# Optimization experiments

Measured on AMD Instinct MI355X. Metric: run time of the kernel, lower is better.

Reference implementation:

```python
import jax, jax.numpy as jnp
import numpy as np

N_NODES = 50000
N_EDGES = 600000
IN_DIM = 9
HID = 128
OUT_DIM = 6


def _mlp2(x, W1, b1, W2, b2):
    # Linear -> ReLU -> Linear
    h = jax.nn.relu(x @ W1 + b1)
    return h @ W2 + b2


def setup_inputs() -> dict:
    key = jax.random.key(0)
    ks = jax.random.split(key, 16)

    def lin(k, fan_in, fan_out):
        # torch nn.Linear default init: U(-1/sqrt(fan_in), 1/sqrt(fan_in))
        bound = 1.0 / np.sqrt(fan_in)
        kw, kb = jax.random.split(k)
        W = jax.random.uniform(kw, (fan_in, fan_out), jnp.float32, -bound, bound)
        b = jax.random.uniform(kb, (fan_out,), jnp.float32, -bound, bound)
        return W, b

    node_states = jax.random.normal(ks[0], (N_NODES, IN_DIM), jnp.float32)
    edge_index = jax.random.randint(ks[1], (2, N_EDGES), 0, N_NODES, jnp.int64 if jax.config.jax_enable_x64 else jnp.int32)
    edge_attr = jax.random.uniform(ks[2], (N_EDGES, 1), jnp.float32)

    ne_W1, ne_b1 = lin(ks[3], IN_DIM, HID)
    ne_W2, ne_b2 = lin(ks[4], HID, HID)
    ee_W1, ee_b1 = lin(ks[5], 2 * HID + 1, HID)
    ee_W2, ee_b2 = lin(ks[6], HID, HID)
    nu_W1, nu_b1 = lin(ks[7], 2 * HID, HID)
    nu_W2, nu_b2 = lin(ks[8], HID, OUT_DIM)

    return {
        "node_states": node_states, "edge_index": edge_index, "edge_attr": edge_attr,
        "ne_W1": ne_W1, "ne_b1": ne_b1, "ne_W2": ne_W2, "ne_b2": ne_b2,
        "ee_W1": ee_W1, "ee_b1": ee_b1, "ee_W2": ee_W2, "ee_b2": ee_b2,
        "nu_W1": nu_W1, "nu_b1": nu_b1, "nu_W2": nu_W2, "nu_b2": nu_b2,
    }


def reference(node_states, edge_index, edge_attr,
              ne_W1, ne_b1, ne_W2, ne_b2,
              ee_W1, ee_b1, ee_W2, ee_b2,
              nu_W1, nu_b1, nu_W2, nu_b2):
    num_nodes = node_states.shape[0]
    # node encoder: [N, 9] -> [N, 128]
    h_v = _mlp2(node_states, ne_W1, ne_b1, ne_W2, ne_b2)

    row, col = edge_index[0], edge_index[1]
    # gather endpoints + concat edge features: [E, 257]
    edge_inputs = jnp.concatenate([h_v[row], h_v[col], edge_attr], axis=1)
    h_e = _mlp2(edge_inputs, ee_W1, ee_b1, ee_W2, ee_b2)  # [E, 128]

    # scatter-add messages to destination nodes (index_add_ on col)
    agg_messages = jax.ops.segment_sum(h_e, col, num_segments=num_nodes)  # [N, 128]

    node_inputs = jnp.concatenate([h_v, agg_messages], axis=1)  # [N, 256]
    gnn_deltas = _mlp2(node_inputs, nu_W1, nu_b1, nu_W2, nu_b2)  # [N, 6]
    return gnn_deltas
```

## Files before the change

kernel.cpp:

```cpp
#include <hip/hip_runtime.h>

#define N_NODES 50000
#define N_EDGES 600000
#define IN_DIM 9
#define HID 128
#define OUT_DIM 6
#define SCAN_BLKS ((N_NODES + 255) / 256)

typedef __attribute__((ext_vector_type(8))) short short8;
typedef __attribute__((ext_vector_type(4))) float f32x4;

__device__ __forceinline__ void split_bf16(float x, ushort& hi, ushort& lo) {
    unsigned u = __float_as_uint(x);
    unsigned r = u + 0x7FFF + ((u >> 16) & 1);
    hi = (ushort)(r >> 16);
    float hif = __uint_as_float((unsigned)hi << 16);
    lo = (ushort)(__float_as_uint(x - hif) >> 16);
}

__global__ __launch_bounds__(128)
void node_encoder(const float* __restrict__ x,
                  const float* __restrict__ W1, const float* __restrict__ b1,
                  const float* __restrict__ W2, const float* __restrict__ b2,
                  ushort* __restrict__ hvh, ushort* __restrict__ hvl)
{
    const int t  = threadIdx.x;
    const int n0 = blockIdx.x * 4;

    __shared__ float xs[4][12];
    __shared__ float h1[4][132];

    if (t < 4 * IN_DIM) {
        int n = t / IN_DIM, k = t % IN_DIM;
        xs[n][k] = x[(n0 + n) * IN_DIM + k];
    }
    __syncthreads();

    float w[IN_DIM];
#pragma unroll
    for (int k = 0; k < IN_DIM; ++k) w[k] = W1[k * HID + t];
    const float bb1 = b1[t];
#pragma unroll
    for (int n = 0; n < 4; ++n) {
        float s = bb1;
#pragma unroll
        for (int k = 0; k < IN_DIM; ++k) s += xs[n][k] * w[k];
        h1[n][t] = fmaxf(s, 0.f);
    }
    __syncthreads();

    float acc[4] = {0.f, 0.f, 0.f, 0.f};
    for (int k = 0; k < HID; k += 4) {
        const float w0 = W2[(k + 0) * HID + t];
        const float w1 = W2[(k + 1) * HID + t];
        const float w2 = W2[(k + 2) * HID + t];
        const float w3 = W2[(k + 3) * HID + t];
#pragma unroll
        for (int n = 0; n < 4; ++n) {
            const float4 a = *(const float4*)&h1[n][k];
            acc[n] += a.x * w0 + a.y * w1 + a.z * w2 + a.w * w3;
        }
    }
    const float bb2 = b2[t];
#pragma unroll
    for (int n = 0; n < 4; ++n) {
        ushort hi, lo;
        split_bf16(acc[n] + bb2, hi, lo);
        hvh[(size_t)(n0 + n) * HID + t] = hi;
        hvl[(size_t)(n0 + n) * HID + t] = lo;
    }
}

__global__ __launch_bounds__(256)
void csr_count(const int* __restrict__ col, int* __restrict__ cnt) {
    const int i = blockIdx.x * 256 + threadIdx.x;
    if (i < N_EDGES) atomicAdd(&cnt[col[i]], 1);
}

__global__ __launch_bounds__(256)
void scan_part(const int* __restrict__ cnt, int* __restrict__ part) {
    __shared__ int s[256];
    const int tid = threadIdx.x;
    const int i = blockIdx.x * 256 + tid;
    s[tid] = (i < N_NODES) ? cnt[i] : 0;
    __syncthreads();
#pragma unroll
    for (int off = 128; off > 0; off >>= 1) {
        if (tid < off) s[tid] += s[tid + off];
        __syncthreads();
    }
    if (tid == 0) part[blockIdx.x] = s[0];
}

__global__ __launch_bounds__(256)
void scan_scan(int* __restrict__ part) {
    __shared__ int s[256];
    const int tid = threadIdx.x;
    const int v = (tid < SCAN_BLKS) ? part[tid] : 0;
    s[tid] = v;
    __syncthreads();
    for (int off = 1; off < 256; off <<= 1) {
        int x = (tid >= off) ? s[tid - off] : 0;
        __syncthreads();
        s[tid] += x;
        __syncthreads();
    }
    part[tid] = s[tid] - v;
}

__global__ __launch_bounds__(256)
void scan_final(const int* __restrict__ cnt, const int* __restrict__ part,
                int* __restrict__ ofs, int* __restrict__ cursor) {
    __shared__ int s[256];
    const int tid = threadIdx.x;
    const int i = blockIdx.x * 256 + tid;
    const int v = (i < N_NODES) ? cnt[i] : 0;
    s[tid] = v;
    __syncthreads();
    for (int off = 1; off < 256; off <<= 1) {
        int x = (tid >= off) ? s[tid - off] : 0;
        __syncthreads();
        s[tid] += x;
        __syncthreads();
    }
    const int excl = part[blockIdx.x] + s[tid] - v;
    if (i <= N_NODES) ofs[i] = excl;
    if (i <  N_NODES) cursor[i] = excl;
}

__global__ __launch_bounds__(256)
void csr_fill(const int* __restrict__ col, int* __restrict__ cursor,
              int* __restrict__ eid) {
    const int i = blockIdx.x * 256 + threadIdx.x;
    if (i < N_EDGES) {
        const int p = atomicAdd(&cursor[col[i]], 1);
        eid[p] = i;
    }
}

__global__ __launch_bounds__(64)
void pack_weights(const float* __restrict__ W1, const float* __restrict__ W2,
                  ushort* __restrict__ p1h, ushort* __restrict__ p1l,
                  ushort* __restrict__ p2h, ushort* __restrict__ p2l)
{
    const int l = threadIdx.x;
    const int b = blockIdx.x;
    if (b < 64) {
        const int kt = b >> 3, nt = b & 7;
        const int kbase = kt * 32 + 8 * (l >> 4);
        const int n = nt * 16 + (l & 15);
#pragma unroll
        for (int j = 0; j < 8; ++j) {
            ushort hi, lo;
            split_bf16(W1[(kbase + j) * HID + n], hi, lo);
            p1h[(b * 64 + l) * 8 + j] = hi;
            p1l[(b * 64 + l) * 8 + j] = lo;
        }
    } else {
        const int u = b - 64;
        const int kt = u >> 3, nt = u & 7;
        const int kbase = kt * 32 + 8 * (l >> 4);
        const int n = nt * 16 + (l & 15);
#pragma unroll
        for (int j = 0; j < 8; ++j) {
            ushort hi, lo;
            split_bf16(W2[(kbase + j) * HID + n], hi, lo);
            p2h[(u * 64 + l) * 8 + j] = hi;
            p2l[(u * 64 + l) * 8 + j] = lo;
        }
    }
}

__global__ __launch_bounds__(256, 8)
void edge_mfma(const ushort* __restrict__ hvh, const ushort* __restrict__ hvl,
               const int* __restrict__ row, const int* __restrict__ col,
               const float* __restrict__ eattr,
               const int* __restrict__ eids,
               const ushort* __restrict__ p1h, const ushort* __restrict__ p1l,
               const ushort* __restrict__ p2h, const ushort* __restrict__ p2l,
               const float* __restrict__ W1,
               const float* __restrict__ b1, const float* __restrict__ b2,
               float* __restrict__ agg)
{
    __shared__ __align__(16) ushort H1h[4096];
    __shared__ __align__(16) ushort H1l[4096];
    __shared__ int   rows_s[32], cols_s[32];
    __shared__ float attr_s[32];

    const int tid = threadIdx.x;
    const int e0  = blockIdx.x * 32;

    if (tid < 32) {
        const int e = eids[e0 + tid];
        rows_s[tid] = row[e];
        cols_s[tid] = col[e];
        attr_s[tid] = eattr[e];
    }
    __syncthreads();

    const int l  = tid & 63;
    const int w  = tid >> 6;
    const int h  = w & 1;
    const int nh = w >> 1;
    const int gl = l >> 4;
    const int r  = l & 15;

    const int edge  = h * 16 + r;
    const int rbyte = rows_s[edge] * 256 + gl * 16;
    const int cbyte = cols_s[edge] * 256 + gl * 16;

    f32x4 acc[4] = {{0,0,0,0},{0,0,0,0},{0,0,0,0},{0,0,0,0}};
#pragma unroll
    for (int kt = 0; kt < 8; ++kt) {
        const int off = (kt < 4) ? (rbyte + kt * 64) : (cbyte + (kt - 4) * 64);
        const short8 ah = *(const short8*)((const char*)hvh + off);
        const short8 al = *(const short8*)((const char*)hvl + off);
#pragma unroll
        for (int i = 0; i < 4; ++i) {
            const int nt = nh * 4 + i;
            const short8 bh = *(const short8*)&p1h[((kt * 8 + nt) * 64 + l) * 8];
            const short8 bl = *(const short8*)&p1l[((kt * 8 + nt) * 64 + l) * 8];
            acc[i] = __builtin_amdgcn_mfma_f32_16x16x32_bf16(ah, bh, acc[i], 0, 0, 0);
            acc[i] = __builtin_amdgcn_mfma_f32_16x16x32_bf16(ah, bl, acc[i], 0, 0, 0);
            acc[i] = __builtin_amdgcn_mfma_f32_16x16x32_bf16(al, bh, acc[i], 0, 0, 0);
        }
    }

#pragma unroll
    for (int i = 0; i < 4; ++i) {
        const int ncol = nh * 64 + i * 16 + r;
        const float w256 = W1[256 * HID + ncol];
        const float bb   = b1[ncol];
        const int kt2 = ncol >> 5;
        const int g2  = (ncol >> 3) & 3;
        const int j   = ncol & 7;
#pragma unroll
        for (int q = 0; q < 4; ++q) {
            const int er = gl * 4 + q;
            const float a = attr_s[h * 16 + er];
            float v = fmaxf(acc[i][q] + bb + a * w256, 0.f);
            ushort hi, lo;
            split_bf16(v, hi, lo);
            const int cell = (kt2 * 2 + h) * 64 + g2 * 16 + er;
            H1h[cell * 8 + j] = hi;
            H1l[cell * 8 + j] = lo;
        }
    }
    __syncthreads();

    f32x4 acc2[4] = {{0,0,0,0},{0,0,0,0},{0,0,0,0},{0,0,0,0}};
#pragma unroll
    for (int kt = 0; kt < 4; ++kt) {
        const short8 ah = *(const short8*)&H1h[((kt * 2 + h) * 64 + l) * 8];
        const short8 al = *(const short8*)&H1l[((kt * 2 + h) * 64 + l) * 8];
#pragma unroll
        for (int i = 0; i < 4; ++i) {
            const int nt = nh * 4 + i;
            const short8 bh = *(const short8*)&p2h[((kt * 8 + nt) * 64 + l) * 8];
            const short8 bl = *(const short8*)&p2l[((kt * 8 + nt) * 64 + l) * 8];
            acc2[i] = __builtin_amdgcn_mfma_f32_16x16x32_bf16(ah, bh, acc2[i], 0, 0, 0);
            acc2[i] = __builtin_amdgcn_mfma_f32_16x16x32_bf16(ah, bl, acc2[i], 0, 0, 0);
            acc2[i] = __builtin_amdgcn_mfma_f32_16x16x32_bf16(al, bh, acc2[i], 0, 0, 0);
        }
    }

    const int er0 = h * 16 + gl * 4;
    const int n0s = cols_s[er0 + 0];
    const int n1s = cols_s[er0 + 1];
    const int n2s = cols_s[er0 + 2];
    const int n3s = cols_s[er0 + 3];
#pragma unroll
    for (int i = 0; i < 4; ++i) {
        const int ncol = nh * 64 + i * 16 + r;
        const float bb = b2[ncol];
        const float v0 = acc2[i][0] + bb;
        const float v1 = acc2[i][1] + bb;
        const float v2 = acc2[i][2] + bb;
        const float v3 = acc2[i][3] + bb;
        if (n0s == n3s) {
            atomicAdd(&agg[(size_t)n0s * HID + ncol], v0 + v1 + v2 + v3);
        } else {
            atomicAdd(&agg[(size_t)n0s * HID + ncol], v0);
            atomicAdd(&agg[(size_t)n1s * HID + ncol], v1);
            atomicAdd(&agg[(size_t)n2s * HID + ncol], v2);
            atomicAdd(&agg[(size_t)n3s * HID + ncol], v3);
        }
    }
}

__global__ __launch_bounds__(128)
void node_update(const ushort* __restrict__ hvh, const ushort* __restrict__ hvl,
                 const float* __restrict__ agg,
                 const float* __restrict__ W1, const float* __restrict__ b1,
                 const float* __restrict__ W2, const float* __restrict__ b2,
                 float* __restrict__ out)
{
    const int t  = threadIdx.x;
    const int n0 = blockIdx.x * 4;

    __shared__ float ins[4][260];
    __shared__ float h1[4][132];
    __shared__ float part[4][2][6];

#pragma unroll
    for (int n = 0; n < 4; ++n) {
        const unsigned hh = hvh[(size_t)(n0 + n) * HID + t];
        const unsigned ll = hvl[(size_t)(n0 + n) * HID + t];
        ins[n][t]       = __uint_as_float(hh << 16) + __uint_as_float(ll << 16);
        ins[n][HID + t] = agg[(size_t)(n0 + n) * HID + t];
    }
    __syncthreads();

    float acc[4] = {0.f, 0.f, 0.f, 0.f};
    for (int k = 0; k < 2 * HID; k += 4) {
        const float w0 = W1[(k + 0) * HID + t];
        const float w1 = W1[(k + 1) * HID + t];
        const float w2 = W1[(k + 2) * HID + t];
        const float w3 = W1[(k + 3) * HID + t];
#pragma unroll
        for (int n = 0; n < 4; ++n) {
            const float4 a = *(const float4*)&ins[n][k];
            acc[n] += a.x * w0 + a.y * w1 + a.z * w2 + a.w * w3;
        }
    }
    const float bb1 = b1[t];
#pragma unroll
    for (int n = 0; n < 4; ++n) h1[n][t] = fmaxf(acc[n] + bb1, 0.f);
    __syncthreads();

    float wv[6];
#pragma unroll
    for (int j = 0; j < 6; ++j) wv[j] = W2[t * OUT_DIM + j];

#pragma unroll
    for (int n = 0; n < 4; ++n) {
        const float v = h1[n][t];
        float p[6];
#pragma unroll
        for (int j = 0; j < 6; ++j) p[j] = v * wv[j];
#pragma unroll
        for (int off = 32; off > 0; off >>= 1) {
#pragma unroll
            for (int j = 0; j < 6; ++j) p[j] += __shfl_down(p[j], off);
        }
        if ((t & 63) == 0) {
#pragma unroll
            for (int j = 0; j < 6; ++j) part[n][t >> 6][j] = p[j];
        }
    }
    __syncthreads();

    if (t < 24) {
        const int n = t / 6, j = t % 6;
        out[(size_t)(n0 + n) * OUT_DIM + j] = part[n][0][j] + part[n][1][j] + b2[j];
    }
}

extern "C" void kernel_launch(void* const* d_in, const int* in_sizes, int n_in,
                              void* d_out, int out_size, void* d_ws, size_t ws_size,
                              hipStream_t stream) {
    const float* node_states = (const float*)d_in[0];
    const int*   edge_index  = (const int*)d_in[1];
    const float* edge_attr   = (const float*)d_in[2];
    const float* ne_W1 = (const float*)d_in[3];
    const float* ne_b1 = (const float*)d_in[4];
    const float* ne_W2 = (const float*)d_in[5];
    const float* ne_b2 = (const float*)d_in[6];
    const float* ee_W1 = (const float*)d_in[7];
    const float* ee_b1 = (const float*)d_in[8];
    const float* ee_W2 = (const float*)d_in[9];
    const float* ee_b2 = (const float*)d_in[10];
    const float* nu_W1 = (const float*)d_in[11];
    const float* nu_b1 = (const float*)d_in[12];
    const float* nu_W2 = (const float*)d_in[13];
    const float* nu_b2 = (const float*)d_in[14];

    const int* row = edge_index;
    const int* col = edge_index + N_EDGES;

    ushort* hvh   = (ushort*)d_ws;
    ushort* hvl   = hvh + (size_t)N_NODES * HID;
    float*  agg   = (float*)(hvl + (size_t)N_NODES * HID);
    int*   cnt    = (int*)(agg + (size_t)N_NODES * HID);
    int*   ofs    = cnt + N_NODES;
    int*   cursor = ofs + (N_NODES + 1);
    int*   partb  = cursor + N_NODES;
    int*   eids   = partb + 256;
    ushort* p1h   = (ushort*)(((uintptr_t)(eids + N_EDGES) + 15) & ~(uintptr_t)15);
    ushort* p1l   = p1h + 32768;
    ushort* p2h   = p1l + 32768;
    ushort* p2l   = p2h + 16384;

    hipMemsetAsync(agg, 0, (size_t)N_NODES * HID * sizeof(float), stream);
    hipMemsetAsync(cnt, 0, N_NODES * sizeof(int), stream);

    node_encoder<<<N_NODES / 4, 128, 0, stream>>>(
        node_states, ne_W1, ne_b1, ne_W2, ne_b2, hvh, hvl);

    csr_count<<<(N_EDGES + 255) / 256, 256, 0, stream>>>(col, cnt);
    scan_part<<<SCAN_BLKS, 256, 0, stream>>>(cnt, partb);
    scan_scan<<<1, 256, 0, stream>>>(partb);
    scan_final<<<SCAN_BLKS, 256, 0, stream>>>(cnt, partb, ofs, cursor);
    csr_fill<<<(N_EDGES + 255) / 256, 256, 0, stream>>>(col, cursor, eids);

    pack_weights<<<96, 64, 0, stream>>>(ee_W1, ee_W2, p1h, p1l, p2h, p2l);

    edge_mfma<<<N_EDGES / 32, 256, 0, stream>>>(
        hvh, hvl, row, col, edge_attr, eids,
        p1h, p1l, p2h, p2l, ee_W1, ee_b1, ee_b2, agg);

    node_update<<<N_NODES / 4, 128, 0, stream>>>(
        hvh, hvl, agg, nu_W1, nu_b1, nu_W2, nu_b2, (float*)d_out);
}
```

Measured before the change: 699.4 us.

## Process 64 edges per block with each wave covering all M-tiles

The edge MLP kernel now handles 64 edges per block instead of 32. Each wave computes 4 M-tiles by 2 N-tiles rather than 1 by 4, so every B-fragment of packed weights loaded from global is reused across four edge tiles, which cuts redundant weight traffic per edge. In exchange the block uses twice the shared memory and more accumulator registers, and the occupancy hint drops from 8 to 4 blocks per CU. The grid size is halved to match.

```diff
diff --git a/kernel.cpp b/kernel.cpp
--- a/kernel.cpp
+++ b/kernel.cpp
@@ -171,7 +171,7 @@
     }
 }
 
-__global__ __launch_bounds__(256, 8)
+__global__ __launch_bounds__(256, 4)
 void edge_mfma(const ushort* __restrict__ hvh, const ushort* __restrict__ hvl,
                const int* __restrict__ row, const int* __restrict__ col,
                const float* __restrict__ eattr,
@@ -182,15 +182,15 @@
                const float* __restrict__ b1, const float* __restrict__ b2,
                float* __restrict__ agg)
 {
-    __shared__ __align__(16) ushort H1h[4096];
-    __shared__ __align__(16) ushort H1l[4096];
-    __shared__ int   rows_s[32], cols_s[32];
-    __shared__ float attr_s[32];
+    __shared__ __align__(16) ushort H1h[8192];
+    __shared__ __align__(16) ushort H1l[8192];
+    __shared__ int   rows_s[64], cols_s[64];
+    __shared__ float attr_s[64];
 
     const int tid = threadIdx.x;
-    const int e0  = blockIdx.x * 32;
-
-    if (tid < 32) {
+    const int e0  = blockIdx.x * 64;
+
+    if (tid < 64) {
         const int e = eids[e0 + tid];
         rows_s[tid] = row[e];
         cols_s[tid] = col[e];
@@ -200,90 +200,113 @@
 
     const int l  = tid & 63;
     const int w  = tid >> 6;
-    const int h  = w & 1;
-    const int nh = w >> 1;
     const int gl = l >> 4;
     const int r  = l & 15;
 
-    const int edge  = h * 16 + r;
-    const int rbyte = rows_s[edge] * 256 + gl * 16;
-    const int cbyte = cols_s[edge] * 256 + gl * 16;
-
-    f32x4 acc[4] = {{0,0,0,0},{0,0,0,0},{0,0,0,0},{0,0,0,0}};
+    int abase[4][2];
+#pragma unroll
+    for (int mt = 0; mt < 4; ++mt) {
+        const int el = mt * 16 + r;
+        abase[mt][0] = rows_s[el] * 256 + gl * 16;
+        abase[mt][1] = cols_s[el] * 256 + gl * 16;
+    }
+
+    f32x4 acc[4][2] = {};
 #pragma unroll
     for (int kt = 0; kt < 8; ++kt) {
-        const int off = (kt < 4) ? (rbyte + kt * 64) : (cbyte + (kt - 4) * 64);
-        const short8 ah = *(const short8*)((const char*)hvh + off);
-        const short8 al = *(const short8*)((const char*)hvl + off);
-#pragma unroll
-        for (int i = 0; i < 4; ++i) {
-            const int nt = nh * 4 + i;
+        const int sel = kt >> 2;
+        const int ko  = (kt & 3) * 64;
+        short8 ah[4], al[4];
+#pragma unroll
+        for (int mt = 0; mt < 4; ++mt) {
+            const int off = abase[mt][sel] + ko;
+            ah[mt] = *(const short8*)((const char*)hvh + off);
+            al[mt] = *(const short8*)((const char*)hvl + off);
+        }
+#pragma unroll
+        for (int i = 0; i < 2; ++i) {
+            const int nt = w * 2 + i;
             const short8 bh = *(const short8*)&p1h[((kt * 8 + nt) * 64 + l) * 8];
             const short8 bl = *(const short8*)&p1l[((kt * 8 + nt) * 64 + l) * 8];
-            acc[i] = __builtin_amdgcn_mfma_f32_16x16x32_bf16(ah, bh, acc[i], 0, 0, 0);
-            acc[i] = __builtin_amdgcn_mfma_f32_16x16x32_bf16(ah, bl, acc[i], 0, 0, 0);
-            acc[i] = __builtin_amdgcn_mfma_f32_16x16x32_bf16(al, bh, acc[i], 0, 0, 0);
-        }
-    }
-
-#pragma unroll
-    for (int i = 0; i < 4; ++i) {
-        const int ncol = nh * 64 + i * 16 + r;
+#pragma unroll
+            for (int mt = 0; mt < 4; ++mt) {
+                acc[mt][i] = __builtin_amdgcn_mfma_f32_16x16x32_bf16(ah[mt], bh, acc[mt][i], 0, 0, 0);
+                acc[mt][i] = __builtin_amdgcn_mfma_f32_16x16x32_bf16(ah[mt], bl, acc[mt][i], 0, 0, 0);
+                acc[mt][i] = __builtin_amdgcn_mfma_f32_16x16x32_bf16(al[mt], bh, acc[mt][i], 0, 0, 0);
+            }
+        }
+    }
+
+#pragma unroll
+    for (int i = 0; i < 2; ++i) {
+        const int ncol = w * 32 + i * 16 + r;
         const float w256 = W1[256 * HID + ncol];
         const float bb   = b1[ncol];
         const int kt2 = ncol >> 5;
-        const int g2  = (ncol >> 3) & 3;
+        const int gg  = (ncol >> 3) & 3;
         const int j   = ncol & 7;
 #pragma unroll
-        for (int q = 0; q < 4; ++q) {
-            const int er = gl * 4 + q;
-            const float a = attr_s[h * 16 + er];
-            float v = fmaxf(acc[i][q] + bb + a * w256, 0.f);
-            ushort hi, lo;
-            split_bf16(v, hi, lo);
-            const int cell = (kt2 * 2 + h) * 64 + g2 * 16 + er;
-            H1h[cell * 8 + j] = hi;
-            H1l[cell * 8 + j] = lo;
-        }
-    }
-    __syncthreads();
-
-    f32x4 acc2[4] = {{0,0,0,0},{0,0,0,0},{0,0,0,0},{0,0,0,0}};
+        for (int mt = 0; mt < 4; ++mt) {
+#pragma unroll
+            for (int q = 0; q < 4; ++q) {
+                const int el = mt * 16 + gl * 4 + q;
+                float v = fmaxf(acc[mt][i][q] + bb + attr_s[el] * w256, 0.f);
+                ushort hi, lo;
+                split_bf16(v, hi, lo);
+                const int cell = (kt2 * 4 + mt) * 64 + gg * 16 + (gl * 4 + q);
+                H1h[cell * 8 + j] = hi;
+                H1l[cell * 8 + j] = lo;
+            }
+        }
+    }
+    __syncthreads();
+
+    f32x4 acc2[4][2] = {};
 #pragma unroll
     for (int kt = 0; kt < 4; ++kt) {
-        const short8 ah = *(const short8*)&H1h[((kt * 2 + h) * 64 + l) * 8];
-        const short8 al = *(const short8*)&H1l[((kt * 2 + h) * 64 + l) * 8];
-#pragma unroll
-        for (int i = 0; i < 4; ++i) {
-            const int nt = nh * 4 + i;
+        short8 ah[4], al[4];
+#pragma unroll
+        for (int mt = 0; mt < 4; ++mt) {
+            ah[mt] = *(const short8*)&H1h[((kt * 4 + mt) * 64 + l) * 8];
+            al[mt] = *(const short8*)&H1l[((kt * 4 + mt) * 64 + l) * 8];
+        }
+#pragma unroll
+        for (int i = 0; i < 2; ++i) {
+            const int nt = w * 2 + i;
             const short8 bh = *(const short8*)&p2h[((kt * 8 + nt) * 64 + l) * 8];
             const short8 bl = *(const short8*)&p2l[((kt * 8 + nt) * 64 + l) * 8];
-            acc2[i] = __builtin_amdgcn_mfma_f32_16x16x32_bf16(ah, bh, acc2[i], 0, 0, 0);
-            acc2[i] = __builtin_amdgcn_mfma_f32_16x16x32_bf16(ah, bl, acc2[i], 0, 0, 0);
-            acc2[i] = __builtin_amdgcn_mfma_f32_16x16x32_bf16(al, bh, acc2[i], 0, 0, 0);
-        }
-    }
-
-    const int er0 = h * 16 + gl * 4;
-    const int n0s = cols_s[er0 + 0];
-    const int n1s = cols_s[er0 + 1];
-    const int n2s = cols_s[er0 + 2];
-    const int n3s = cols_s[er0 + 3];
-#pragma unroll
-    for (int i = 0; i < 4; ++i) {
-        const int ncol = nh * 64 + i * 16 + r;
-        const float bb = b2[ncol];
-        const float v0 = acc2[i][0] + bb;
-        const float v1 = acc2[i][1] + bb;
-        const float v2 = acc2[i][2] + bb;
-        const float v3 = acc2[i][3] + bb;
-        if (n0s == n3s) {
-            atomicAdd(&agg[(size_t)n0s * HID + ncol], v0 + v1 + v2 + v3);
-        } else {
-            atomicAdd(&agg[(size_t)n0s * HID + ncol], v0);
-            atomicAdd(&agg[(size_t)n1s * HID + ncol], v1);
-            atomicAdd(&agg[(size_t)n2s * HID + ncol], v2);
-            atomicAdd(&agg[(size_t)n3s * HID + ncol], v3);
+#pragma unroll
+            for (int mt = 0; mt < 4; ++mt) {
+                acc2[mt][i] = __builtin_amdgcn_mfma_f32_16x16x32_bf16(ah[mt], bh, acc2[mt][i], 0, 0, 0);
+                acc2[mt][i] = __builtin_amdgcn_mfma_f32_16x16x32_bf16(ah[mt], bl, acc2[mt][i], 0, 0, 0);
+                acc2[mt][i] = __builtin_amdgcn_mfma_f32_16x16x32_bf16(al[mt], bh, acc2[mt][i], 0, 0, 0);
+            }
+        }
+    }
+
+#pragma unroll
+    for (int mt = 0; mt < 4; ++mt) {
+        const int er0 = mt * 16 + gl * 4;
+        const int n0s = cols_s[er0 + 0];
+        const int n3s = cols_s[er0 + 3];
+        const int n1s = cols_s[er0 + 1];
+        const int n2s = cols_s[er0 + 2];
+#pragma unroll
+        for (int i = 0; i < 2; ++i) {
+            const int ncol = w * 32 + i * 16 + r;
+            const float bb = b2[ncol];
+            const float v0 = acc2[mt][i][0] + bb;
+            const float v1 = acc2[mt][i][1] + bb;
+            const float v2 = acc2[mt][i][2] + bb;
+            const float v3 = acc2[mt][i][3] + bb;
+            if (n0s == n3s) {
+                atomicAdd(&agg[(size_t)n0s * HID + ncol], v0 + v1 + v2 + v3);
+            } else {
+                atomicAdd(&agg[(size_t)n0s * HID + ncol], v0);
+                atomicAdd(&agg[(size_t)n1s * HID + ncol], v1);
+                atomicAdd(&agg[(size_t)n2s * HID + ncol], v2);
+                atomicAdd(&agg[(size_t)n3s * HID + ncol], v3);
+            }
         }
     }
 }
@@ -405,7 +428,7 @@
 
     pack_weights<<<96, 64, 0, stream>>>(ee_W1, ee_W2, p1h, p1l, p2h, p2l);
 
-    edge_mfma<<<N_EDGES / 32, 256, 0, stream>>>(
+    edge_mfma<<<N_EDGES / 64, 256, 0, stream>>>(
         hvh, hvl, row, col, edge_attr, eids,
         p1h, p1l, p2h, p2l, ee_W1, ee_b1, ee_b2, agg);
 
```

After: 645.3 us. 1.08x faster.
